# Kernel optimization log

Hardware: AMD Instinct MI355X
Metric: run time of the kernel (lower is better)

The kernel has to match this reference:

```python
import jax, jax.numpy as jnp
import numpy as np

B, S, D = 2, 2048, 1024
H = 16
HD = D // H
SCALE = HD ** (-0.5)


def setup_inputs() -> dict:
    key = jax.random.key(0)
    k1, k2, k3, k4 = jax.random.split(key, 4)
    x = jax.random.normal(k1, (B, S, D), dtype=jnp.float32)
    # nn.Linear-style init scale to keep activations sane
    w_qkv = jax.random.normal(k2, (3 * D, D), dtype=jnp.float32) * (D ** -0.5)
    w_out = jax.random.normal(k3, (D, D), dtype=jnp.float32) * (D ** -0.5)
    b_out = jax.random.normal(k4, (D,), dtype=jnp.float32) * 0.01
    return {"x": x, "w_qkv": w_qkv, "w_out": w_out, "b_out": b_out}


def reference(x, w_qkv, w_out, b_out):
    b, s, d = x.shape
    # qkv projection (no bias): [b, s, 3d]
    qkv = jnp.einsum('bsd,ed->bse', x, w_qkv)
    # Rearrange 'b c (e h hd) -> e b h c hd'
    qkv = qkv.reshape(b, s, 3, H, HD).transpose(2, 0, 3, 1, 4)
    # NOTE: original splits as (v, q, k) in that order
    v, q, k = qkv[0], qkv[1], qkv[2]
    # scale applied after matmul, as in the original
    scores = jnp.einsum('bhqd,bhkd->bhqk', q, k) * SCALE
    attn = jax.nn.softmax(scores, axis=-1)
    o = jnp.einsum('bhqk,bhkd->bhqd', attn, v)
    # 'b h c hd -> b c (h hd)'
    o = o.transpose(0, 2, 1, 3).reshape(b, s, d)
    return jnp.einsum('bsd,ed->bse', o, w_out) + b_out
```

## Files before the change

### kernel.cpp

```cpp
#include <hip/hip_runtime.h>
#include <cstdint>
#include <cstddef>

#define BB 2
#define SS 2048
#define DD 1024
#define HH 16
#define HDIM 64

typedef short bf16x8 __attribute__((ext_vector_type(8)));
typedef short bf16x4 __attribute__((ext_vector_type(4)));
typedef float f32x4 __attribute__((ext_vector_type(4)));
typedef float f32x2 __attribute__((ext_vector_type(2)));

union U4S8 { uint4 u; bf16x8 s; };
union U2S4 { uint2 u; bf16x4 s; unsigned short h[4]; };

#if defined(__HIP_DEVICE_COMPILE__)
# if __has_builtin(__builtin_amdgcn_exp2f)
#  define EXP2(x) __builtin_amdgcn_exp2f(x)
# else
#  define EXP2(x) exp2f(x)
# endif
#else
# define EXP2(x) exp2f(x)
#endif

__device__ __forceinline__ unsigned short f2bf(float f) {
    union { float f; unsigned int u; } c; c.f = f;
    unsigned int u = c.u;
    unsigned int r = (u + 0x7FFFu + ((u >> 16) & 1u)) >> 16;
    return (unsigned short)r;
}

__device__ __forceinline__ void async_cp16(const void* g, void* l) {
    __builtin_amdgcn_global_load_lds(
        (const __attribute__((address_space(1))) void*)g,
        (__attribute__((address_space(3))) void*)l, 16, 0, 0);
}

__global__ __launch_bounds__(256) void cvt_all(
    const float* __restrict__ x, const float* __restrict__ wq,
    const float* __restrict__ wo,
    unsigned short* __restrict__ xb, unsigned short* __restrict__ wqb,
    unsigned short* __restrict__ wob) {
    int i = blockIdx.x * 256 + threadIdx.x;
    const float* in; unsigned short* out; int j;
    if (i < 524288)       { in = x;  out = xb;  j = i; }
    else if (i < 917504)  { in = wq; out = wqb; j = i - 524288; }
    else                  { in = wo; out = wob; j = i - 917504; }
    float4 a = ((const float4*)in)[2 * j];
    float4 b = ((const float4*)in)[2 * j + 1];
    union { uint4 u; unsigned short h[8]; } o;
    o.h[0] = f2bf(a.x); o.h[1] = f2bf(a.y); o.h[2] = f2bf(a.z); o.h[3] = f2bf(a.w);
    o.h[4] = f2bf(b.x); o.h[5] = f2bf(b.y); o.h[6] = f2bf(b.z); o.h[7] = f2bf(b.w);
    ((uint4*)out)[j] = o.u;
}

__global__ __launch_bounds__(512, 2) void gemm_qkv(
    const unsigned short* __restrict__ A,
    const unsigned short* __restrict__ Bw,
    unsigned short* __restrict__ qb, unsigned short* __restrict__ kb,
    unsigned short* __restrict__ vb) {
    const int K = 1024;
    __shared__ unsigned short smem[65536];
    int tid = threadIdx.x;
    int lane = tid & 63, wave = tid >> 6;
    int wmp = wave & 1, wnp = wave >> 1;
    int lm = lane & 15, lq = lane >> 4;

    int id = blockIdx.y * 12 + blockIdx.x;
    int swz = (id & 7) * 24 + (id >> 3);
    int m0 = (swz / 12) * 256, n0 = (swz % 12) * 256;

    f32x4 acc[8][4] = {};

    int u2 = tid >> 2;
    int c2 = (tid & 3) ^ (u2 & 3);
    int sdst = tid * 8;
    const unsigned short* gA0 = A  + (size_t)(m0 + u2) * K + c2 * 8;
    const unsigned short* gB0 = Bw + (size_t)(n0 + u2) * K + c2 * 8;
    const unsigned short* gA1 = gA0 + (size_t)128 * K;
    const unsigned short* gB1 = gB0 + (size_t)128 * K;

#define STAGE4(j, kk) do {                                                  \
        async_cp16(gA0 + (kk), smem + (j) * 16384 + 0     + sdst);          \
        async_cp16(gA1 + (kk), smem + (j) * 16384 + 4096  + sdst);          \
        async_cp16(gB0 + (kk), smem + (j) * 16384 + 8192  + sdst);          \
        async_cp16(gB1 + (kk), smem + (j) * 16384 + 12288 + sdst);          \
    } while (0)

    int axk = (lq ^ (lm & 3)) * 8;
    int aBase = (wmp * 128 + lm) * 32 + axk;
    int bBase = 8192 + (wnp * 64 + lm) * 32 + axk;
    U4S8 af[8], bfr[4];

#define KT(j, kk3) do {                                                     \
        _Pragma("unroll")                                                   \
        for (int m = 0; m < 8; m++)                                         \
            af[m].u = *(const uint4*)(smem + (j) * 16384 + aBase + m * 512);\
        _Pragma("unroll")                                                   \
        for (int n = 0; n < 4; n++)                                         \
            bfr[n].u = *(const uint4*)(smem + (j) * 16384 + bBase + n * 512);\
        STAGE4((((j) + 3) & 3), kk3);                                       \
        _Pragma("unroll")                                                   \
        for (int m = 0; m < 8; m++)                                         \
            _Pragma("unroll")                                               \
            for (int n = 0; n < 4; n++)                                     \
                acc[m][n] = __builtin_amdgcn_mfma_f32_16x16x32_bf16(        \
                    af[m].s, bfr[n].s, acc[m][n], 0, 0, 0);                 \
        asm volatile("s_waitcnt vmcnt(8)" ::: "memory");                    \
        __builtin_amdgcn_s_barrier();                                       \
    } while (0)

    STAGE4(0, 0); STAGE4(1, 32); STAGE4(2, 64);
    asm volatile("s_waitcnt vmcnt(8)" ::: "memory");
    __builtin_amdgcn_s_barrier();

    #pragma unroll 1
    for (int t4 = 0; t4 < 8; ++t4) {
        int kb128 = t4 * 128;
        KT(0, kb128 + 96);
        KT(1, kb128 + 128);
        KT(2, kb128 + 160);
        KT(3, kb128 + 192);
    }
#undef KT
#undef STAGE4

    asm volatile("s_waitcnt vmcnt(0)" ::: "memory");
    __builtin_amdgcn_s_barrier();

    unsigned short* Lw = smem + wave * 8192;
    int wm = wmp * 128, wn = wnp * 64;
    int b = m0 >> 11;
    int s_base = (m0 + wm) & 2047;
    int h = ((n0 + wn) >> 6) & 15;
    if (n0 < 1024) {
        unsigned short* vdst = vb + ((size_t)(b * HH + h) * HDIM) * SS;
        #pragma unroll
        for (int c = 0; c < 2; c++) {
            #pragma unroll
            for (int m4 = 0; m4 < 4; m4++)
                #pragma unroll
                for (int ni = 0; ni < 4; ni++) {
                    U2S4 t;
                    #pragma unroll
                    for (int r = 0; r < 4; r++)
                        t.h[r] = f2bf(acc[c * 4 + m4][ni][r]);
                    *(uint2*)&Lw[(ni * 16 + lm) * 72 + m4 * 16 + lq * 4] = t.u;
                }
            __builtin_amdgcn_wave_barrier();
            #pragma unroll
            for (int it = 0; it < 8; it++) {
                int hd = it * 8 + (lane >> 3);
                int so = (lane & 7) * 8;
                uint4 val = *(const uint4*)&Lw[hd * 72 + so];
                *(uint4*)(vdst + (size_t)hd * SS + s_base + c * 64 + so) = val;
            }
            __builtin_amdgcn_wave_barrier();
        }
    } else {
        bool isq = n0 < 2048;
        unsigned short* dst = isq ? qb : kb;
        float scale = isq ? 0.18033688f : 1.0f;
        unsigned short* qdst = dst + ((size_t)(b * HH + h) * SS) * HDIM;
        #pragma unroll
        for (int c = 0; c < 2; c++) {
            #pragma unroll
            for (int m4 = 0; m4 < 4; m4++)
                #pragma unroll
                for (int ni = 0; ni < 4; ni++)
                    #pragma unroll
                    for (int r = 0; r < 4; r++)
                        Lw[(m4 * 16 + lq * 4 + r) * 72 + ni * 16 + lm] =
                            f2bf(acc[c * 4 + m4][ni][r] * scale);
            __builtin_amdgcn_wave_barrier();
            #pragma unroll
            for (int it = 0; it < 8; it++) {
                int srw = it * 8 + (lane >> 3);
                int so = (lane & 7) * 8;
                uint4 val = *(const uint4*)&Lw[srw * 72 + so];
                *(uint4*)(qdst + (size_t)(s_base + c * 64 + srw) * HDIM + so) = val;
            }
            __builtin_amdgcn_wave_barrier();
        }
    }
}

__global__ __launch_bounds__(512) void attn(
    const unsigned short* __restrict__ qb,
    const unsigned short* __restrict__ kb,
    const unsigned short* __restrict__ vb,
    unsigned short* __restrict__ ob) {
    int bh = blockIdx.y;
    int q0 = blockIdx.x * 128;
    int tid = threadIdx.x, lane = tid & 63, wave = tid >> 6;
    int grp = wave >> 2;
    int w4  = wave & 3;
    int lm = lane & 15, lq = lane >> 4;

    __shared__ unsigned short smem[65536];
    float* smf = (float*)smem;

    const unsigned short* qg = qb + (size_t)bh * SS * HDIM;
    const unsigned short* kg = kb + (size_t)bh * SS * HDIM;
    const unsigned short* vg = vb + (size_t)bh * HDIM * SS;

    U4S8 qf[2][2];
    #pragma unroll
    for (int qt = 0; qt < 2; qt++)
        #pragma unroll
        for (int ks = 0; ks < 2; ks++)
            qf[qt][ks].u = *(const uint4*)(
                qg + (size_t)(q0 + w4 * 32 + qt * 16 + lm) * HDIM + ks * 32 + lq * 8);

    f32x4 oacc[4][2] = {};
    f32x2 lsum2[2] = {};

    int lm7 = lm & 7;
    int kidx = lm * 64 + 8 * (lq ^ lm7);
    int vidx[2];
    #pragma unroll
    for (int kblk = 0; kblk < 2; kblk++)
        vidx[kblk] = lm * 64 + 8 * (((kblk << 2) | lq) ^ lm7);

    int sr  = tid >> 3;
    int s5  = sr & 31;
    int kap = (sr & 32) + (((s5 >> 2) & 3) << 3) + (((s5 >> 4) & 1) << 2) + (s5 & 3);
    int lch = (tid & 7) ^ (sr & 7);
    int sdst = tid * 8;
    const unsigned short* kpA = kg + (size_t)kap * HDIM + lch * 8;
    const unsigned short* kpB = kpA + 64 * HDIM;
    const unsigned short* vpA = vg + (size_t)sr * SS + lch * 8;
    const unsigned short* vpB = vpA + 64;

    #define STAGE(pbase)                                                       \
        do {                                                                   \
            async_cp16(kpA, smem + (pbase) + sdst);                            \
            async_cp16(kpB, smem + (pbase) + 4096 + sdst);                     \
            async_cp16(vpA, smem + (pbase) + 8192 + sdst);                     \
            async_cp16(vpB, smem + (pbase) + 12288 + sdst);                    \
            kpA += 128 * HDIM; kpB += 128 * HDIM; vpA += 128; vpB += 128;      \
        } while (0)

    STAGE(0); STAGE(16384); STAGE(32768);
    asm volatile("s_waitcnt vmcnt(8)" ::: "memory");
    __builtin_amdgcn_s_barrier();

    #pragma unroll 1
    for (int t = 0; t < 16; ++t) {
        int cb = (t & 3) << 14;
        STAGE(((t + 3) & 3) << 14);

        int kbase = cb + grp * 4096;
        int vbase = cb + 8192 + grp * 4096;

        U4S8 pb8[2][2];
        #pragma unroll
        for (int mi = 0; mi < 4; mi++) {
            U4S8 kf0, kf1;
            kf0.u = *(const uint4*)(smem + kbase + mi * 1024 + kidx);
            kf1.u = *(const uint4*)(smem + kbase + mi * 1024 + (kidx ^ 32));
            #pragma unroll
            for (int qt = 0; qt < 2; qt++) {
                f32x4 sa = {};
                sa = __builtin_amdgcn_mfma_f32_16x16x32_bf16(kf0.s, qf[qt][0].s, sa, 0, 0, 0);
                sa = __builtin_amdgcn_mfma_f32_16x16x32_bf16(kf1.s, qf[qt][1].s, sa, 0, 0, 0);
                float p0 = EXP2(sa[0]);
                float p1 = EXP2(sa[1]);
                float p2 = EXP2(sa[2]);
                float p3 = EXP2(sa[3]);
                f32x2 a01; a01[0] = p0; a01[1] = p1;
                f32x2 a23; a23[0] = p2; a23[1] = p3;
                lsum2[qt] += a01;
                lsum2[qt] += a23;
                unsigned int lo, hi;
                asm("v_cvt_pk_bf16_f32 %0, %1, %2" : "=v"(lo) : "v"(p0), "v"(p1));
                asm("v_cvt_pk_bf16_f32 %0, %1, %2" : "=v"(hi) : "v"(p2), "v"(p3));
                if ((mi & 1) == 0) { pb8[mi >> 1][qt].u.x = lo; pb8[mi >> 1][qt].u.y = hi; }
                else               { pb8[mi >> 1][qt].u.z = lo; pb8[mi >> 1][qt].u.w = hi; }
            }
        }

        #pragma unroll
        for (int mi2 = 0; mi2 < 4; mi2++) {
            #pragma unroll
            for (int kblk = 0; kblk < 2; kblk++) {
                U4S8 vf;
                vf.u = *(const uint4*)(smem + vbase + mi2 * 1024 + vidx[kblk]);
                oacc[mi2][0] = __builtin_amdgcn_mfma_f32_16x16x32_bf16(
                    vf.s, pb8[kblk][0].s, oacc[mi2][0], 0, 0, 0);
                oacc[mi2][1] = __builtin_amdgcn_mfma_f32_16x16x32_bf16(
                    vf.s, pb8[kblk][1].s, oacc[mi2][1], 0, 0, 0);
            }
        }

        asm volatile("s_waitcnt vmcnt(8)" ::: "memory");
        __builtin_amdgcn_s_barrier();
    }
    #undef STAGE

    float gsum[2];
    #pragma unroll
    for (int qt = 0; qt < 2; qt++) {
        float s = lsum2[qt][0] + lsum2[qt][1];
        s += __shfl_xor(s, 16);
        s += __shfl_xor(s, 32);
        gsum[qt] = s;
    }

    asm volatile("s_waitcnt vmcnt(0)" ::: "memory");
    __syncthreads();

    if (grp == 1) {
        float* pub = smf + w4 * 2048;
        #pragma unroll
        for (int mi2 = 0; mi2 < 4; mi2++)
            #pragma unroll
            for (int qt = 0; qt < 2; qt++)
                #pragma unroll
                for (int r = 0; r < 4; r++)
                    pub[(mi2 * 8 + qt * 4 + r) * 64 + lane] = oacc[mi2][qt][r];
        if (lq == 0) {
            smf[8192 + w4 * 32 + lm]      = gsum[0];
            smf[8192 + w4 * 32 + 16 + lm] = gsum[1];
        }
    }
    __syncthreads();

    if (grp == 0) {
        float* pub = smf + w4 * 2048;
        #pragma unroll
        for (int mi2 = 0; mi2 < 4; mi2++)
            #pragma unroll
            for (int qt = 0; qt < 2; qt++)
                #pragma unroll
                for (int r = 0; r < 4; r++)
                    oacc[mi2][qt][r] += pub[(mi2 * 8 + qt * 4 + r) * 64 + lane];
        float inv[2];
        inv[0] = 1.f / (gsum[0] + smf[8192 + w4 * 32 + lm]);
        inv[1] = 1.f / (gsum[1] + smf[8192 + w4 * 32 + 16 + lm]);

        unsigned short* Ow = smem + 17024 + w4 * 2304;
        #pragma unroll
        for (int mi2 = 0; mi2 < 4; mi2++)
            #pragma unroll
            for (int qt = 0; qt < 2; qt++) {
                U2S4 t;
                #pragma unroll
                for (int r = 0; r < 4; r++)
                    t.h[r] = f2bf(oacc[mi2][qt][r] * inv[qt]);
                *(uint2*)&Ow[(qt * 16 + lm) * 72 + mi2 * 16 + lq * 4] = t.u;
            }
        __builtin_amdgcn_wave_barrier();
        int b = bh >> 4, h = bh & 15;
        #pragma unroll
        for (int it = 0; it < 4; it++) {
            int q  = it * 8 + (lane >> 3);
            int off = (lane & 7) * 8;
            uint4 val = *(const uint4*)&Ow[q * 72 + off];
            int srw = q0 + w4 * 32 + q;
            *(uint4*)(ob + (size_t)(b * SS + srw) * DD + h * 64 + off) = val;
        }
    }
}

__global__ __launch_bounds__(256) void gemm_out(
    const unsigned short* __restrict__ A,
    const unsigned short* __restrict__ Bw,
    const float* __restrict__ bias, float* __restrict__ out) {
    const int K = 1024;
    __shared__ unsigned short smem[24576];
    int tid = threadIdx.x;
    int lane = tid & 63, wave = tid >> 6;
    int wm = (wave & 1) * 64, wn = (wave >> 1) * 32;
    int m0 = blockIdx.y * 128, n0 = blockIdx.x * 64;
    int lm = lane & 15, lq = lane >> 4;

    f32x4 acc[4][2] = {};

    int sdst = tid * 8;
    int lch = (tid & 3) ^ ((tid >> 3) & 3);
    const unsigned short* gA = A  + (size_t)(m0 + (tid >> 2)) * K + lch * 8;
    const unsigned short* gB = Bw + (size_t)(n0 + (tid >> 2)) * K + lch * 8;
    int sw = (lq ^ ((lm >> 1) & 3)) * 8;

#define OSTAGE(k0, buf) do {                                               \
        async_cp16(gA + (k0),               smem + (buf) + sdst);          \
        async_cp16(gA + 64 * K + (k0),      smem + (buf) + 2048 + sdst);   \
        async_cp16(gA + (k0) + 32,          smem + (buf) + 4096 + sdst);   \
        async_cp16(gA + 64 * K + (k0) + 32, smem + (buf) + 6144 + sdst);   \
        async_cp16(gB + (k0),               smem + (buf) + 8192 + sdst);   \
        async_cp16(gB + (k0) + 32,          smem + (buf) + 10240 + sdst);  \
    } while (0)

    OSTAGE(0, 0);
    for (int k0 = 0; k0 < K; k0 += 128) {
        #pragma unroll
        for (int hf = 0; hf < 2; hf++) {
            int base = hf ? 12288 : 0;
            int obuf = hf ? 0 : 12288;
            __syncthreads();
            int kn = k0 + 64 + hf * 64;
            if (kn < K) OSTAGE(kn, obuf);
            #pragma unroll
            for (int kc = 0; kc < 2; kc++) {
                const unsigned short* As = smem + base + kc * 4096;
                const unsigned short* Bs = smem + base + 8192 + kc * 2048;
                U4S8 af[4], bfx[2];
                #pragma unroll
                for (int i = 0; i < 4; i++)
                    af[i].u = *(const uint4*)(As + (wm + i * 16 + lm) * 32 + sw);
                #pragma unroll
                for (int i = 0; i < 2; i++)
                    bfx[i].u = *(const uint4*)(Bs + (wn + i * 16 + lm) * 32 + sw);
                #pragma unroll
                for (int mi = 0; mi < 4; mi++)
                    #pragma unroll
                    for (int ni = 0; ni < 2; ni++)
                        acc[mi][ni] = __builtin_amdgcn_mfma_f32_16x16x32_bf16(
                            af[mi].s, bfx[ni].s, acc[mi][ni], 0, 0, 0);
            }
        }
    }
#undef OSTAGE

    #pragma unroll
    for (int mi = 0; mi < 4; mi++) {
        int gr = m0 + wm + mi * 16 + lq * 4;
        #pragma unroll
        for (int ni = 0; ni < 2; ni++) {
            int gc = n0 + wn + ni * 16 + lm;
            float bv = bias[gc];
            #pragma unroll
            for (int r = 0; r < 4; r++)
                out[(size_t)(gr + r) * DD + gc] = acc[mi][ni][r] + bv;
        }
    }
}

extern "C" void kernel_launch(void* const* d_in, const int* in_sizes, int n_in,
                              void* d_out, int out_size, void* d_ws, size_t ws_size,
                              hipStream_t stream) {
    const float* x     = (const float*)d_in[0];
    const float* w_qkv = (const float*)d_in[1];
    const float* w_out = (const float*)d_in[2];
    const float* b_out = (const float*)d_in[3];
    float* out = (float*)d_out;

    unsigned short* ws = (unsigned short*)d_ws;
    const size_t NX = (size_t)BB * SS * DD;
    unsigned short* x_bf    = ws;
    unsigned short* wqkv_bf = x_bf + NX;
    unsigned short* wout_bf = wqkv_bf + 3145728;
    unsigned short* q_buf   = wout_bf + 1048576;
    unsigned short* k_buf   = q_buf + NX;
    unsigned short* v_buf   = k_buf + NX;
    unsigned short* o_buf   = v_buf + NX;

    cvt_all<<<4096, 256, 0, stream>>>(x, w_qkv, w_out, x_bf, wqkv_bf, wout_bf);
    gemm_qkv<<<dim3(12, 16), 512, 0, stream>>>(x_bf, wqkv_bf, q_buf, k_buf, v_buf);
    attn<<<dim3(16, 32), 512, 0, stream>>>(q_buf, k_buf, v_buf, o_buf);
    gemm_out<<<dim3(16, 32), 256, 0, stream>>>(o_buf, wout_bf, b_out, out);
}
```

Measured before the change: 185.6 us.

## Double-buffer attention K/V staging and deepen output GEMM pipeline to four stages

The attention kernel drops its four-slot async K/V ring with explicit vmcnt waits and switches to a two-buffer ping-pong synchronised with __syncthreads. This halves its shared memory, which could let two blocks fit per CU. The output projection GEMM goes the other way: it moves from a double-buffered 64-wide K step to a four-slot ring of 32-wide K tiles, waiting with vmcnt(6) and a barrier, and gets a simpler swizzle. The trade is less prefetch depth in attention for more occupancy, while the GEMM gets more copy/compute overlap.

Result: faster. 172.1 us (-7.3%).

```diff
diff --git a/kernel.cpp b/kernel.cpp
--- a/kernel.cpp
+++ b/kernel.cpp
@@ -200,7 +200,7 @@
     int w4  = wave & 3;
     int lm = lane & 15, lq = lane >> 4;
 
-    __shared__ unsigned short smem[65536];
+    __shared__ unsigned short smem[32768];
     float* smf = (float*)smem;
 
     const unsigned short* qg = qb + (size_t)bh * SS * HDIM;
@@ -244,60 +244,59 @@
             kpA += 128 * HDIM; kpB += 128 * HDIM; vpA += 128; vpB += 128;      \
         } while (0)
 
-    STAGE(0); STAGE(16384); STAGE(32768);
-    asm volatile("s_waitcnt vmcnt(8)" ::: "memory");
-    __builtin_amdgcn_s_barrier();
-
-    #pragma unroll 1
-    for (int t = 0; t < 16; ++t) {
-        int cb = (t & 3) << 14;
-        STAGE(((t + 3) & 3) << 14);
-
-        int kbase = cb + grp * 4096;
-        int vbase = cb + 8192 + grp * 4096;
-
-        U4S8 pb8[2][2];
-        #pragma unroll
-        for (int mi = 0; mi < 4; mi++) {
-            U4S8 kf0, kf1;
-            kf0.u = *(const uint4*)(smem + kbase + mi * 1024 + kidx);
-            kf1.u = *(const uint4*)(smem + kbase + mi * 1024 + (kidx ^ 32));
-            #pragma unroll
-            for (int qt = 0; qt < 2; qt++) {
-                f32x4 sa = {};
-                sa = __builtin_amdgcn_mfma_f32_16x16x32_bf16(kf0.s, qf[qt][0].s, sa, 0, 0, 0);
-                sa = __builtin_amdgcn_mfma_f32_16x16x32_bf16(kf1.s, qf[qt][1].s, sa, 0, 0, 0);
-                float p0 = EXP2(sa[0]);
-                float p1 = EXP2(sa[1]);
-                float p2 = EXP2(sa[2]);
-                float p3 = EXP2(sa[3]);
-                f32x2 a01; a01[0] = p0; a01[1] = p1;
-                f32x2 a23; a23[0] = p2; a23[1] = p3;
-                lsum2[qt] += a01;
-                lsum2[qt] += a23;
-                unsigned int lo, hi;
-                asm("v_cvt_pk_bf16_f32 %0, %1, %2" : "=v"(lo) : "v"(p0), "v"(p1));
-                asm("v_cvt_pk_bf16_f32 %0, %1, %2" : "=v"(hi) : "v"(p2), "v"(p3));
-                if ((mi & 1) == 0) { pb8[mi >> 1][qt].u.x = lo; pb8[mi >> 1][qt].u.y = hi; }
-                else               { pb8[mi >> 1][qt].u.z = lo; pb8[mi >> 1][qt].u.w = hi; }
+    STAGE(0);
+
+    for (int kt = 0; kt < SS / 128; kt += 2) {
+        #pragma unroll
+        for (int hf = 0; hf < 2; hf++) {
+            int cbase = hf ? 16384 : 0;
+            int obase = hf ? 0 : 16384;
+            __syncthreads();
+            STAGE(obase);
+
+            int kbase = cbase + grp * 4096;
+            int vbase = cbase + 8192 + grp * 4096;
+
+            U4S8 pb8[2][2];
+            #pragma unroll
+            for (int mi = 0; mi < 4; mi++) {
+                U4S8 kf0, kf1;
+                kf0.u = *(const uint4*)(smem + kbase + mi * 1024 + kidx);
+                kf1.u = *(const uint4*)(smem + kbase + mi * 1024 + (kidx ^ 32));
+                #pragma unroll
+                for (int qt = 0; qt < 2; qt++) {
+                    f32x4 sa = {};
+                    sa = __builtin_amdgcn_mfma_f32_16x16x32_bf16(kf0.s, qf[qt][0].s, sa, 0, 0, 0);
+                    sa = __builtin_amdgcn_mfma_f32_16x16x32_bf16(kf1.s, qf[qt][1].s, sa, 0, 0, 0);
+                    float p0 = EXP2(sa[0]);
+                    float p1 = EXP2(sa[1]);
+                    float p2 = EXP2(sa[2]);
+                    float p3 = EXP2(sa[3]);
+                    f32x2 a01; a01[0] = p0; a01[1] = p1;
+                    f32x2 a23; a23[0] = p2; a23[1] = p3;
+                    lsum2[qt] += a01;
+                    lsum2[qt] += a23;
+                    unsigned int lo, hi;
+                    asm("v_cvt_pk_bf16_f32 %0, %1, %2" : "=v"(lo) : "v"(p0), "v"(p1));
+                    asm("v_cvt_pk_bf16_f32 %0, %1, %2" : "=v"(hi) : "v"(p2), "v"(p3));
+                    if ((mi & 1) == 0) { pb8[mi >> 1][qt].u.x = lo; pb8[mi >> 1][qt].u.y = hi; }
+                    else               { pb8[mi >> 1][qt].u.z = lo; pb8[mi >> 1][qt].u.w = hi; }
+                }
             }
-        }
-
-        #pragma unroll
-        for (int mi2 = 0; mi2 < 4; mi2++) {
-            #pragma unroll
-            for (int kblk = 0; kblk < 2; kblk++) {
-                U4S8 vf;
-                vf.u = *(const uint4*)(smem + vbase + mi2 * 1024 + vidx[kblk]);
-                oacc[mi2][0] = __builtin_amdgcn_mfma_f32_16x16x32_bf16(
-                    vf.s, pb8[kblk][0].s, oacc[mi2][0], 0, 0, 0);
-                oacc[mi2][1] = __builtin_amdgcn_mfma_f32_16x16x32_bf16(
-                    vf.s, pb8[kblk][1].s, oacc[mi2][1], 0, 0, 0);
+
+            #pragma unroll
+            for (int mi2 = 0; mi2 < 4; mi2++) {
+                #pragma unroll
+                for (int kblk = 0; kblk < 2; kblk++) {
+                    U4S8 vf;
+                    vf.u = *(const uint4*)(smem + vbase + mi2 * 1024 + vidx[kblk]);
+                    oacc[mi2][0] = __builtin_amdgcn_mfma_f32_16x16x32_bf16(
+                        vf.s, pb8[kblk][0].s, oacc[mi2][0], 0, 0, 0);
+                    oacc[mi2][1] = __builtin_amdgcn_mfma_f32_16x16x32_bf16(
+                        vf.s, pb8[kblk][1].s, oacc[mi2][1], 0, 0, 0);
+                }
             }
         }
-
-        asm volatile("s_waitcnt vmcnt(8)" ::: "memory");
-        __builtin_amdgcn_s_barrier();
     }
     #undef STAGE
 
@@ -310,7 +309,6 @@
         gsum[qt] = s;
     }
 
-    asm volatile("s_waitcnt vmcnt(0)" ::: "memory");
     __syncthreads();
 
     if (grp == 1) {
@@ -380,51 +378,51 @@
 
     f32x4 acc[4][2] = {};
 
+    int u = tid >> 2;
+    int c2 = (tid & 3) ^ (u & 3);
     int sdst = tid * 8;
-    int lch = (tid & 3) ^ ((tid >> 3) & 3);
-    const unsigned short* gA = A  + (size_t)(m0 + (tid >> 2)) * K + lch * 8;
-    const unsigned short* gB = Bw + (size_t)(n0 + (tid >> 2)) * K + lch * 8;
-    int sw = (lq ^ ((lm >> 1) & 3)) * 8;
-
-#define OSTAGE(k0, buf) do {                                               \
-        async_cp16(gA + (k0),               smem + (buf) + sdst);          \
-        async_cp16(gA + 64 * K + (k0),      smem + (buf) + 2048 + sdst);   \
-        async_cp16(gA + (k0) + 32,          smem + (buf) + 4096 + sdst);   \
-        async_cp16(gA + 64 * K + (k0) + 32, smem + (buf) + 6144 + sdst);   \
-        async_cp16(gB + (k0),               smem + (buf) + 8192 + sdst);   \
-        async_cp16(gB + (k0) + 32,          smem + (buf) + 10240 + sdst);  \
+    const unsigned short* gA0 = A  + (size_t)(m0 + u) * K + c2 * 8;
+    const unsigned short* gA1 = gA0 + (size_t)64 * K;
+    const unsigned short* gB0 = Bw + (size_t)(n0 + u) * K + c2 * 8;
+
+#define OSTG(j, kk) do {                                                   \
+        async_cp16(gA0 + (kk), smem + (j) * 6144 + sdst);                  \
+        async_cp16(gA1 + (kk), smem + (j) * 6144 + 2048 + sdst);           \
+        async_cp16(gB0 + (kk), smem + (j) * 6144 + 4096 + sdst);           \
     } while (0)
 
-    OSTAGE(0, 0);
-    for (int k0 = 0; k0 < K; k0 += 128) {
-        #pragma unroll
-        for (int hf = 0; hf < 2; hf++) {
-            int base = hf ? 12288 : 0;
-            int obuf = hf ? 0 : 12288;
-            __syncthreads();
-            int kn = k0 + 64 + hf * 64;
-            if (kn < K) OSTAGE(kn, obuf);
-            #pragma unroll
-            for (int kc = 0; kc < 2; kc++) {
-                const unsigned short* As = smem + base + kc * 4096;
-                const unsigned short* Bs = smem + base + 8192 + kc * 2048;
-                U4S8 af[4], bfx[2];
-                #pragma unroll
-                for (int i = 0; i < 4; i++)
-                    af[i].u = *(const uint4*)(As + (wm + i * 16 + lm) * 32 + sw);
-                #pragma unroll
-                for (int i = 0; i < 2; i++)
-                    bfx[i].u = *(const uint4*)(Bs + (wn + i * 16 + lm) * 32 + sw);
-                #pragma unroll
-                for (int mi = 0; mi < 4; mi++)
-                    #pragma unroll
-                    for (int ni = 0; ni < 2; ni++)
-                        acc[mi][ni] = __builtin_amdgcn_mfma_f32_16x16x32_bf16(
-                            af[mi].s, bfx[ni].s, acc[mi][ni], 0, 0, 0);
-            }
-        }
-    }
-#undef OSTAGE
+    int axk = (lq ^ (lm & 3)) * 8;
+    int aBase = (wm + lm) * 32 + axk;
+    int bBase = 4096 + (wn + lm) * 32 + axk;
+
+    OSTG(0, 0); OSTG(1, 32); OSTG(2, 64);
+    asm volatile("s_waitcnt vmcnt(6)" ::: "memory");
+    __builtin_amdgcn_s_barrier();
+
+    #pragma unroll 1
+    for (int t = 0; t < 32; ++t) {
+        int cb = (t & 3) * 6144;
+        int kks = (t + 3 < 32) ? (t + 3) * 32 : 0;
+        U4S8 af[4], bfx[2];
+        #pragma unroll
+        for (int m = 0; m < 4; m++)
+            af[m].u = *(const uint4*)(smem + cb + aBase + m * 512);
+        #pragma unroll
+        for (int n = 0; n < 2; n++)
+            bfx[n].u = *(const uint4*)(smem + cb + bBase + n * 512);
+        OSTG((t + 3) & 3, kks);
+        #pragma unroll
+        for (int m = 0; m < 4; m++)
+            #pragma unroll
+            for (int n = 0; n < 2; n++)
+                acc[m][n] = __builtin_amdgcn_mfma_f32_16x16x32_bf16(
+                    af[m].s, bfx[n].s, acc[m][n], 0, 0, 0);
+        asm volatile("s_waitcnt vmcnt(6)" ::: "memory");
+        __builtin_amdgcn_s_barrier();
+    }
+#undef OSTG
+
+    asm volatile("s_waitcnt vmcnt(0)" ::: "memory");
 
     #pragma unroll
     for (int mi = 0; mi < 4; mi++) {
```
